# Kernel tuning notes

Hardware: AMD Instinct MI355X
Metric: run time of the kernel (lower is better)

## Reference

```python
import jax, jax.numpy as jnp
import numpy as np
from jax import lax

# QuantumDMRGLayer (isolated_labelnode=True) as a pure MPS chain contraction.
# Per sample: contract each site's (2,m[,m]) tensor with the 2-dim input vector
# over the physical leg, then multiply the resulting bond matrices along the
# chain, inserting the (m,m,nblabels) output tensor after site pos_label.

B, L, M, NBL = 2048, 196, 16, 10  # batch, dimvec, bond_len, nblabels


def setup_inputs() -> dict:
    key = jax.random.key(0)
    k_in, k_mid, k_l, k_r, k_out = jax.random.split(key, 5)
    # std chosen for numerical stability of a 196-long matrix product:
    # each site matrix is x0*A[0]+x1*A[1] with x~N(0,1), so effective per-site
    # gain ~ std*sqrt(2*m); std = 1/sqrt(2*m) keeps the product O(1).
    std = 1.0 / np.sqrt(2.0 * M)
    inputs = jax.random.normal(k_in, (B, L, 2), dtype=jnp.float32)
    eye2m = jnp.eye(M, dtype=jnp.float32)[:2, :]  # eye(max(2,m))[0:2,:] -> (2, m)
    A_left = eye2m + 1e-3 * jax.random.normal(k_l, (2, M), dtype=jnp.float32)
    A_right = eye2m + 1e-3 * jax.random.normal(k_r, (2, M), dtype=jnp.float32)
    A_mid = std * jax.random.normal(k_mid, (L - 2, 2, M, M), dtype=jnp.float32)
    T_out = (1.0 / np.sqrt(M)) * jax.random.normal(k_out, (M, M, NBL), dtype=jnp.float32)
    return {
        "inputs": inputs,
        "A_left": A_left,
        "A_mid": A_mid,
        "A_right": A_right,
        "T_out": T_out,
        "pos_label": 98,
    }


def reference(inputs, A_left, A_mid, A_right, T_out, pos_label):
    # Contract physical legs: interior site i (1..L-2) -> batched (m,m) matrix.
    mats = jnp.einsum("bsd,sdij->sbij", inputs[:, 1:-1, :], A_mid)  # (L-2, B, m, m)
    v_left = jnp.einsum("bd,dm->bm", inputs[:, 0, :], A_left)       # (B, m)
    v_right = jnp.einsum("bd,dm->bm", inputs[:, -1, :], A_right)    # (B, m)

    def step_l(v, Mx):  # v @ M, batched
        return jnp.einsum("bm,bmn->bn", v, Mx), None

    def step_r(v, Mx):  # M @ v, batched (sweep from the right end inward)
        return jnp.einsum("bmn,bn->bm", Mx, v), None

    # sites 1..pos_label feed the left bond of the output node,
    # sites pos_label+1..L-2 feed the right bond.
    left, _ = lax.scan(step_l, v_left, mats[:pos_label])
    right, _ = lax.scan(step_r, v_right, mats[pos_label:], reverse=True)
    return jnp.einsum("bm,mnl,bn->bl", left, T_out, right)  # (B, nblabels)
```

## Files before the change

kernel.cpp:

```cpp
#include <hip/hip_runtime.h>


typedef __attribute__((ext_vector_type(8))) short short8;
typedef __attribute__((ext_vector_type(16))) float floatx16;

#define GSITE_DW 512
#define GDIR_DW (100 * GSITE_DW)
#define STATE_DW (2 * GDIR_DW)

__device__ __forceinline__ unsigned bf16_rne(unsigned u) {
    return (u + 0x7FFFu + ((u >> 16) & 1u)) >> 16;
}

__global__ __launch_bounds__(256)
void prep_kernel(const float* __restrict__ AM, unsigned* __restrict__ WS)
{
    const int bid = blockIdx.x;
    const int dir = bid / 100;
    const int p   = bid % 100;
    const int lim = dir ? 96 : 98;
    const int a   = dir ? (193 - p) : p;
    const int t   = threadIdx.x;

    __shared__ float sM[512];
    if (p < lim)
        ((float2*)sM)[t] = ((const float2*)(AM + a * 512))[t];
    else
        ((float2*)sM)[t] = make_float2(0.f, 0.f);
    __syncthreads();

    const int w    = t & 3;
    const int lane = t >> 2;
    const int kb = (lane >> 5) << 3;
    const int r  = lane & 31;
    const int rr = (r & 0x13) | ((r & 4) << 1) | ((r & 8) >> 1);
    const int d = rr >> 4, nn = rr & 15;
    const int k0 = kb + 2 * w;

    float g0, g1;
    if (dir == 0) { g0 = sM[d * 256 + k0 * 16 + nn];
                    g1 = sM[d * 256 + (k0 + 1) * 16 + nn]; }
    else          { g0 = sM[d * 256 + nn * 16 + k0];
                    g1 = sM[d * 256 + nn * 16 + k0 + 1]; }

    const unsigned h0 = bf16_rne(__float_as_uint(g0));
    const unsigned h1 = bf16_rne(__float_as_uint(g1));
    const float l0f = g0 - __uint_as_float(h0 << 16);
    const float l1f = g1 - __uint_as_float(h1 << 16);
    const unsigned lo0 = bf16_rne(__float_as_uint(l0f));
    const unsigned lo1 = bf16_rne(__float_as_uint(l1f));

    unsigned* gp = WS + (dir * 100 + p) * GSITE_DW;
    gp[t]       = (h1 << 16) | h0;
    gp[256 + t] = (lo1 << 16) | lo0;
}

__global__ __launch_bounds__(64, 1)
void chain_kernel(const float* __restrict__ X,
                  const float* __restrict__ AL,
                  const float* __restrict__ AR,
                  const unsigned* __restrict__ WS,
                  float* __restrict__ WST)
{
    const int lane = threadIdx.x;
    const int dir  = blockIdx.x & 1;
    const int s    = (blockIdx.x >> 1) * 32 + (lane & 31);
    const int kb   = (lane >> 5) << 3;
    const float* Xs = X + s * 392;
    const unsigned* Gb = WS + dir * GDIR_DW + lane * 4;

    float w[8];
    int4 vh4, vl4;
    auto pack = [&]() {
#pragma unroll
        for (int q = 0; q < 4; ++q) {
            const unsigned u0 = __float_as_uint(w[2 * q]);
            const unsigned u1 = __float_as_uint(w[2 * q + 1]);
            const float l0 = w[2 * q]     - __uint_as_float(u0 & 0xFFFF0000u);
            const float l1 = w[2 * q + 1] - __uint_as_float(u1 & 0xFFFF0000u);
            ((unsigned*)&vh4)[q] = __builtin_amdgcn_perm(u1, u0, 0x07060302u);
            ((unsigned*)&vl4)[q] = __builtin_amdgcn_perm(
                __float_as_uint(l1), __float_as_uint(l0), 0x07060302u);
        }
    };

    const float* Ai = dir ? AR : AL;
    const float2 xi = *(const float2*)(Xs + (dir ? 390 : 0));
#pragma unroll
    for (int j = 0; j < 8; ++j)
        w[j] = xi.x * Ai[kb + j] + xi.y * Ai[16 + kb + j];
    pack();

    int4 GH[4], GL[4];
    float2 xr[4];
#pragma unroll
    for (int i = 0; i < 4; ++i) {
        GH[i] = *(const int4*)(Gb + i * GSITE_DW);
        GL[i] = *(const int4*)(Gb + i * GSITE_DW + 256);
        xr[i] = *(const float2*)(Xs + (dir ? (388 - 2 * i) : (2 + 2 * i)));
    }

    auto site = [&](int j4, bool pf, int pn) {
        const short8 ah = *(short8*)&GH[j4];
        const short8 al = *(short8*)&GL[j4];
        const short8 bh = *(short8*)&vh4;
        const short8 bl = *(short8*)&vl4;
        floatx16 Da = {}, Db = {};
        Da = __builtin_amdgcn_mfma_f32_32x32x16_bf16(ah, bh, Da, 0, 0, 0);
        Db = __builtin_amdgcn_mfma_f32_32x32x16_bf16(ah, bl, Db, 0, 0, 0);
        Db = __builtin_amdgcn_mfma_f32_32x32x16_bf16(al, bh, Db, 0, 0, 0);
        const float2 xs = xr[j4];
        if (pf) {
            GH[j4] = *(const int4*)(Gb + pn * GSITE_DW);
            GL[j4] = *(const int4*)(Gb + pn * GSITE_DW + 256);
            xr[j4] = *(const float2*)(Xs + (dir ? (388 - 2 * pn)
                                                : (2 + 2 * pn)));
        }
#pragma unroll
        for (int j = 0; j < 8; ++j)
            w[j] = fmaf(xs.x, Da[j] + Db[j], xs.y * (Da[j + 8] + Db[j + 8]));
        pack();
    };

    for (int c = 0; c < 24; ++c) {
#pragma unroll
        for (int j4 = 0; j4 < 4; ++j4)
            site(j4, true, 4 * c + j4 + 4);
    }
    if (dir == 0) {
        site(0, false, 0);
        site(1, false, 0);
    }

    float* st = WST + (dir * 2048 + s) * 16 + kb;
    *(float4*)(st)     = make_float4(w[0], w[1], w[2], w[3]);
    *(float4*)(st + 4) = make_float4(w[4], w[5], w[6], w[7]);
}

__global__ __launch_bounds__(256)
void out_kernel(const float* __restrict__ T, const float* __restrict__ WST,
                float* __restrict__ OUT)
{
    __shared__ float sT[2560];
    const int tid = threadIdx.x;
    for (int k = tid; k < 640; k += 256)
        ((float4*)sT)[k] = ((const float4*)T)[k];
    __syncthreads();
    const int t = blockIdx.x * 256 + tid;
    const int s = t / 10, l = t - s * 10;
    const float* L = WST + s * 16;
    const float* R = WST + 2048 * 16 + s * 16;
    const float4 Ra = *(const float4*)(R);
    const float4 Rb = *(const float4*)(R + 4);
    const float4 Rc = *(const float4*)(R + 8);
    const float4 Rd = *(const float4*)(R + 12);
    float acc = 0.f;
#pragma unroll
    for (int m = 0; m < 16; ++m) {
        const float lm = L[m];
        const float* Tp = sT + m * 160 + l;
        acc = fmaf(lm * Ra.x, Tp[0],   acc);
        acc = fmaf(lm * Ra.y, Tp[10],  acc);
        acc = fmaf(lm * Ra.z, Tp[20],  acc);
        acc = fmaf(lm * Ra.w, Tp[30],  acc);
        acc = fmaf(lm * Rb.x, Tp[40],  acc);
        acc = fmaf(lm * Rb.y, Tp[50],  acc);
        acc = fmaf(lm * Rb.z, Tp[60],  acc);
        acc = fmaf(lm * Rb.w, Tp[70],  acc);
        acc = fmaf(lm * Rc.x, Tp[80],  acc);
        acc = fmaf(lm * Rc.y, Tp[90],  acc);
        acc = fmaf(lm * Rc.z, Tp[100], acc);
        acc = fmaf(lm * Rc.w, Tp[110], acc);
        acc = fmaf(lm * Rd.x, Tp[120], acc);
        acc = fmaf(lm * Rd.y, Tp[130], acc);
        acc = fmaf(lm * Rd.z, Tp[140], acc);
        acc = fmaf(lm * Rd.w, Tp[150], acc);
    }
    OUT[t] = acc;
}

extern "C" void kernel_launch(void* const* d_in, const int* in_sizes, int n_in,
                              void* d_out, int out_size, void* d_ws, size_t ws_size,
                              hipStream_t stream)
{
    const float* X  = (const float*)d_in[0];
    const float* AL = (const float*)d_in[1];
    const float* AM = (const float*)d_in[2];
    const float* AR = (const float*)d_in[3];
    const float* T  = (const float*)d_in[4];
    (void)in_sizes; (void)n_in; (void)out_size; (void)ws_size;
    unsigned* WS = (unsigned*)d_ws;
    float* WST   = (float*)d_ws + STATE_DW;
    float* OUT   = (float*)d_out;

    hipLaunchKernelGGL(prep_kernel,  dim3(200), dim3(256), 0, stream, AM, WS);
    hipLaunchKernelGGL(chain_kernel, dim3(128), dim3(64),  0, stream,
                       X, AL, AR, WS, WST);
    hipLaunchKernelGGL(out_kernel,   dim3(80),  dim3(256), 0, stream,
                       T, WST, OUT);
}
```

Measured before the change: 89.68 us.

## Fuse output contraction into chain kernel and pack both directions per block

Merges the out_kernel into the chain kernel. Each 128-thread block now runs the left and right sweeps for 32 samples as two waves, exchanges the final bond vectors through shared memory, and contracts them with a transposed copy of T staged in LDS. The site update math is rewritten with 2-wide float vectors to encourage packed FMA instructions. This removes one kernel launch and the workspace round trip. In exchange it halves the block count, to 64 CUs with two waves each, and adds a serial epilogue plus T staging to the critical path.

```diff
diff --git a/kernel.cpp b/kernel.cpp
--- a/kernel.cpp
+++ b/kernel.cpp
@@ -3,10 +3,10 @@
 
 typedef __attribute__((ext_vector_type(8))) short short8;
 typedef __attribute__((ext_vector_type(16))) float floatx16;
+typedef __attribute__((ext_vector_type(2))) float float2v;
 
 #define GSITE_DW 512
 #define GDIR_DW (100 * GSITE_DW)
-#define STATE_DW (2 * GDIR_DW)
 
 __device__ __forceinline__ unsigned bf16_rne(unsigned u) {
     return (u + 0x7FFFu + ((u >> 16) & 1u)) >> 16;
@@ -55,41 +55,57 @@
     gp[256 + t] = (lo1 << 16) | lo0;
 }
 
-__global__ __launch_bounds__(64, 1)
+__global__ __launch_bounds__(128, 1)
 void chain_kernel(const float* __restrict__ X,
                   const float* __restrict__ AL,
                   const float* __restrict__ AR,
+                  const float* __restrict__ T,
                   const unsigned* __restrict__ WS,
-                  float* __restrict__ WST)
+                  float* __restrict__ OUT)
 {
-    const int lane = threadIdx.x;
-    const int dir  = blockIdx.x & 1;
-    const int s    = (blockIdx.x >> 1) * 32 + (lane & 31);
+    __shared__ float sTt[2560];
+    __shared__ float sS[2][32][16];
+
+    const int tid  = threadIdx.x;
+    const int dir  = tid >> 6;
+    const int lane = tid & 63;
+    const int sl   = lane & 31;
     const int kb   = (lane >> 5) << 3;
+    const int s    = (int)blockIdx.x * 32 + sl;
     const float* Xs = X + s * 392;
     const unsigned* Gb = WS + dir * GDIR_DW + lane * 4;
 
-    float w[8];
+    for (int k = tid; k < 2560; k += 128) {
+        const int m = k / 160, rem = k - m * 160;
+        const int n = rem / 10, l = rem - n * 10;
+        sTt[l * 256 + m * 16 + n] = T[k];
+    }
+
+    float2v w2[4];
     int4 vh4, vl4;
-    auto pack = [&]() {
+    auto packv = [&]() {
 #pragma unroll
         for (int q = 0; q < 4; ++q) {
-            const unsigned u0 = __float_as_uint(w[2 * q]);
-            const unsigned u1 = __float_as_uint(w[2 * q + 1]);
-            const float l0 = w[2 * q]     - __uint_as_float(u0 & 0xFFFF0000u);
-            const float l1 = w[2 * q + 1] - __uint_as_float(u1 & 0xFFFF0000u);
+            const unsigned u0 = __float_as_uint(w2[q].x);
+            const unsigned u1 = __float_as_uint(w2[q].y);
+            float2v hi;
+            hi.x = __uint_as_float(u0 & 0xFFFF0000u);
+            hi.y = __uint_as_float(u1 & 0xFFFF0000u);
+            const float2v lo = w2[q] - hi;
             ((unsigned*)&vh4)[q] = __builtin_amdgcn_perm(u1, u0, 0x07060302u);
             ((unsigned*)&vl4)[q] = __builtin_amdgcn_perm(
-                __float_as_uint(l1), __float_as_uint(l0), 0x07060302u);
+                __float_as_uint(lo.y), __float_as_uint(lo.x), 0x07060302u);
         }
     };
 
     const float* Ai = dir ? AR : AL;
     const float2 xi = *(const float2*)(Xs + (dir ? 390 : 0));
 #pragma unroll
-    for (int j = 0; j < 8; ++j)
-        w[j] = xi.x * Ai[kb + j] + xi.y * Ai[16 + kb + j];
-    pack();
+    for (int q = 0; q < 4; ++q) {
+        w2[q].x = xi.x * Ai[kb + 2 * q]     + xi.y * Ai[16 + kb + 2 * q];
+        w2[q].y = xi.x * Ai[kb + 2 * q + 1] + xi.y * Ai[16 + kb + 2 * q + 1];
+    }
+    packv();
 
     int4 GH[4], GL[4];
     float2 xr[4];
@@ -116,10 +132,18 @@
             xr[j4] = *(const float2*)(Xs + (dir ? (388 - 2 * pn)
                                                 : (2 + 2 * pn)));
         }
-#pragma unroll
-        for (int j = 0; j < 8; ++j)
-            w[j] = fmaf(xs.x, Da[j] + Db[j], xs.y * (Da[j + 8] + Db[j + 8]));
-        pack();
+        const float2v xx = {xs.x, xs.x}, xy = {xs.y, xs.y};
+#pragma unroll
+        for (int q = 0; q < 4; ++q) {
+            const float2v da = {Da[2 * q],     Da[2 * q + 1]};
+            const float2v db = {Db[2 * q],     Db[2 * q + 1]};
+            const float2v ea = {Da[2 * q + 8], Da[2 * q + 9]};
+            const float2v eb = {Db[2 * q + 8], Db[2 * q + 9]};
+            const float2v s0 = da + db;
+            const float2v s1 = ea + eb;
+            w2[q] = __builtin_elementwise_fma(xx, s0, xy * s1);
+        }
+        packv();
     };
 
     for (int c = 0; c < 24; ++c) {
@@ -132,51 +156,47 @@
         site(1, false, 0);
     }
 
-    float* st = WST + (dir * 2048 + s) * 16 + kb;
-    *(float4*)(st)     = make_float4(w[0], w[1], w[2], w[3]);
-    *(float4*)(st + 4) = make_float4(w[4], w[5], w[6], w[7]);
-}
-
-__global__ __launch_bounds__(256)
-void out_kernel(const float* __restrict__ T, const float* __restrict__ WST,
-                float* __restrict__ OUT)
-{
-    __shared__ float sT[2560];
-    const int tid = threadIdx.x;
-    for (int k = tid; k < 640; k += 256)
-        ((float4*)sT)[k] = ((const float4*)T)[k];
+#pragma unroll
+    for (int q = 0; q < 4; ++q)
+        *(float2*)&sS[dir][sl][kb + 2 * q] = make_float2(w2[q].x, w2[q].y);
     __syncthreads();
-    const int t = blockIdx.x * 256 + tid;
-    const int s = t / 10, l = t - s * 10;
-    const float* L = WST + s * 16;
-    const float* R = WST + 2048 * 16 + s * 16;
-    const float4 Ra = *(const float4*)(R);
-    const float4 Rb = *(const float4*)(R + 4);
-    const float4 Rc = *(const float4*)(R + 8);
-    const float4 Rd = *(const float4*)(R + 12);
-    float acc = 0.f;
-#pragma unroll
-    for (int m = 0; m < 16; ++m) {
-        const float lm = L[m];
-        const float* Tp = sT + m * 160 + l;
-        acc = fmaf(lm * Ra.x, Tp[0],   acc);
-        acc = fmaf(lm * Ra.y, Tp[10],  acc);
-        acc = fmaf(lm * Ra.z, Tp[20],  acc);
-        acc = fmaf(lm * Ra.w, Tp[30],  acc);
-        acc = fmaf(lm * Rb.x, Tp[40],  acc);
-        acc = fmaf(lm * Rb.y, Tp[50],  acc);
-        acc = fmaf(lm * Rb.z, Tp[60],  acc);
-        acc = fmaf(lm * Rb.w, Tp[70],  acc);
-        acc = fmaf(lm * Rc.x, Tp[80],  acc);
-        acc = fmaf(lm * Rc.y, Tp[90],  acc);
-        acc = fmaf(lm * Rc.z, Tp[100], acc);
-        acc = fmaf(lm * Rc.w, Tp[110], acc);
-        acc = fmaf(lm * Rd.x, Tp[120], acc);
-        acc = fmaf(lm * Rd.y, Tp[130], acc);
-        acc = fmaf(lm * Rd.z, Tp[140], acc);
-        acc = fmaf(lm * Rd.w, Tp[150], acc);
-    }
-    OUT[t] = acc;
+
+    for (int o = tid; o < 320; o += 128) {
+        const int sm = o / 10, l = o - sm * 10;
+        const float* L = sS[0][sm];
+        const float* R = sS[1][sm];
+        const float4 Ra = *(const float4*)(R);
+        const float4 Rb = *(const float4*)(R + 4);
+        const float4 Rc = *(const float4*)(R + 8);
+        const float4 Rd = *(const float4*)(R + 12);
+        const float* Tp = sTt + l * 256;
+        float acc = 0.f;
+#pragma unroll
+        for (int m = 0; m < 16; ++m) {
+            const float lm = L[m];
+            const float4 t0 = *(const float4*)(Tp + m * 16);
+            const float4 t1 = *(const float4*)(Tp + m * 16 + 4);
+            const float4 t2 = *(const float4*)(Tp + m * 16 + 8);
+            const float4 t3 = *(const float4*)(Tp + m * 16 + 12);
+            acc = fmaf(lm * Ra.x, t0.x, acc);
+            acc = fmaf(lm * Ra.y, t0.y, acc);
+            acc = fmaf(lm * Ra.z, t0.z, acc);
+            acc = fmaf(lm * Ra.w, t0.w, acc);
+            acc = fmaf(lm * Rb.x, t1.x, acc);
+            acc = fmaf(lm * Rb.y, t1.y, acc);
+            acc = fmaf(lm * Rb.z, t1.z, acc);
+            acc = fmaf(lm * Rb.w, t1.w, acc);
+            acc = fmaf(lm * Rc.x, t2.x, acc);
+            acc = fmaf(lm * Rc.y, t2.y, acc);
+            acc = fmaf(lm * Rc.z, t2.z, acc);
+            acc = fmaf(lm * Rc.w, t2.w, acc);
+            acc = fmaf(lm * Rd.x, t3.x, acc);
+            acc = fmaf(lm * Rd.y, t3.y, acc);
+            acc = fmaf(lm * Rd.z, t3.z, acc);
+            acc = fmaf(lm * Rd.w, t3.w, acc);
+        }
+        OUT[((int)blockIdx.x * 32 + sm) * 10 + l] = acc;
+    }
 }
 
 extern "C" void kernel_launch(void* const* d_in, const int* in_sizes, int n_in,
@@ -190,12 +210,9 @@
     const float* T  = (const float*)d_in[4];
     (void)in_sizes; (void)n_in; (void)out_size; (void)ws_size;
     unsigned* WS = (unsigned*)d_ws;
-    float* WST   = (float*)d_ws + STATE_DW;
     float* OUT   = (float*)d_out;
 
     hipLaunchKernelGGL(prep_kernel,  dim3(200), dim3(256), 0, stream, AM, WS);
-    hipLaunchKernelGGL(chain_kernel, dim3(128), dim3(64),  0, stream,
-                       X, AL, AR, WS, WST);
-    hipLaunchKernelGGL(out_kernel,   dim3(80),  dim3(256), 0, stream,
-                       T, WST, OUT);
-}
+    hipLaunchKernelGGL(chain_kernel, dim3(64),  dim3(128), 0, stream,
+                       X, AL, AR, T, WS, OUT);
+}
```

After: 92.27 us. +2.9%, slower.

## Pre-multiply adjacent site tensors pairwise to halve sequential chain steps

Applied to the files above, without the earlier changes.

The prep kernel now multiplies each pair of adjacent site tensors into four 16x16 products per physical-index combination (d1,d2). The chain then advances two sites per step using six independent MFMAs combined with the outer product of the two input vectors. This halves the length of the serial dependency chain and lets the MFMAs overlap, at the cost of more MFMA work per step, more register traffic, and rounding the fused product to bf16 hi/lo.

```diff
diff --git a/kernel.cpp b/kernel.cpp
--- a/kernel.cpp
+++ b/kernel.cpp
@@ -3,9 +3,10 @@
 
 typedef __attribute__((ext_vector_type(8))) short short8;
 typedef __attribute__((ext_vector_type(16))) float floatx16;
-
-#define GSITE_DW 512
-#define GDIR_DW (100 * GSITE_DW)
+typedef __attribute__((ext_vector_type(2))) float float2v;
+
+#define PAIR_DW 1024
+#define GDIR_DW (50 * PAIR_DW)
 #define STATE_DW (2 * GDIR_DW)
 
 __device__ __forceinline__ unsigned bf16_rne(unsigned u) {
@@ -16,17 +17,23 @@
 void prep_kernel(const float* __restrict__ AM, unsigned* __restrict__ WS)
 {
     const int bid = blockIdx.x;
-    const int dir = bid / 100;
-    const int p   = bid % 100;
-    const int lim = dir ? 96 : 98;
-    const int a   = dir ? (193 - p) : p;
+    const int dir = bid / 50;
+    const int q   = bid % 50;
     const int t   = threadIdx.x;
 
-    __shared__ float sM[512];
-    if (p < lim)
-        ((float2*)sM)[t] = ((const float2*)(AM + a * 512))[t];
-    else
-        ((float2*)sM)[t] = make_float2(0.f, 0.f);
+    __shared__ float sF[512];
+    __shared__ float sS[512];
+
+    int i0, i1; bool valid;
+    if (dir == 0) { i0 = 2 * q;       i1 = 2 * q + 1;   valid = (q < 49); }
+    else          { i0 = 193 - 2 * q; i1 = 192 - 2 * q; valid = (q < 48); }
+    if (valid) {
+        ((float2*)sF)[t] = ((const float2*)(AM + i0 * 512))[t];
+        ((float2*)sS)[t] = ((const float2*)(AM + i1 * 512))[t];
+    } else {
+        ((float2*)sF)[t] = make_float2(0.f, 0.f);
+        ((float2*)sS)[t] = make_float2(0.f, 0.f);
+    }
     __syncthreads();
 
     const int w    = t & 3;
@@ -37,22 +44,49 @@
     const int d = rr >> 4, nn = rr & 15;
     const int k0 = kb + 2 * w;
 
-    float g0, g1;
-    if (dir == 0) { g0 = sM[d * 256 + k0 * 16 + nn];
-                    g1 = sM[d * 256 + (k0 + 1) * 16 + nn]; }
-    else          { g0 = sM[d * 256 + nn * 16 + k0];
-                    g1 = sM[d * 256 + nn * 16 + k0 + 1]; }
-
-    const unsigned h0 = bf16_rne(__float_as_uint(g0));
-    const unsigned h1 = bf16_rne(__float_as_uint(g1));
-    const float l0f = g0 - __uint_as_float(h0 << 16);
-    const float l1f = g1 - __uint_as_float(h1 << 16);
-    const unsigned lo0 = bf16_rne(__float_as_uint(l0f));
-    const unsigned lo1 = bf16_rne(__float_as_uint(l1f));
-
-    unsigned* gp = WS + (dir * 100 + p) * GSITE_DW;
-    gp[t]       = (h1 << 16) | h0;
-    gp[256 + t] = (lo1 << 16) | lo0;
+    float g10 = 0.f, g11 = 0.f, g20 = 0.f, g21 = 0.f;
+    if (dir == 0) {
+#pragma unroll
+        for (int u = 0; u < 16; ++u) {
+            const float s2 = sS[d * 256 + u * 16 + nn];
+            g10 = fmaf(sF[      k0 * 16 + u],       s2, g10);
+            g11 = fmaf(sF[      (k0 + 1) * 16 + u], s2, g11);
+            g20 = fmaf(sF[256 + k0 * 16 + u],       s2, g20);
+            g21 = fmaf(sF[256 + (k0 + 1) * 16 + u], s2, g21);
+        }
+    } else {
+#pragma unroll
+        for (int u = 0; u < 16; ++u) {
+            const float f0 = sF[d * 256 + u * 16 + k0];
+            const float f1 = sF[d * 256 + u * 16 + k0 + 1];
+            const float a0 = sS[      nn * 16 + u];
+            const float a1 = sS[256 + nn * 16 + u];
+            g10 = fmaf(a0, f0, g10);  g11 = fmaf(a0, f1, g11);
+            g20 = fmaf(a1, f0, g20);  g21 = fmaf(a1, f1, g21);
+        }
+    }
+
+    unsigned* gp = WS + (dir * 50 + q) * PAIR_DW;
+    {
+        const unsigned h0 = bf16_rne(__float_as_uint(g10));
+        const unsigned h1 = bf16_rne(__float_as_uint(g11));
+        const unsigned l0 = bf16_rne(__float_as_uint(
+            g10 - __uint_as_float(h0 << 16)));
+        const unsigned l1 = bf16_rne(__float_as_uint(
+            g11 - __uint_as_float(h1 << 16)));
+        gp[t]       = (h1 << 16) | h0;
+        gp[256 + t] = (l1 << 16) | l0;
+    }
+    {
+        const unsigned h0 = bf16_rne(__float_as_uint(g20));
+        const unsigned h1 = bf16_rne(__float_as_uint(g21));
+        const unsigned l0 = bf16_rne(__float_as_uint(
+            g20 - __uint_as_float(h0 << 16)));
+        const unsigned l1 = bf16_rne(__float_as_uint(
+            g21 - __uint_as_float(h1 << 16)));
+        gp[512 + t] = (h1 << 16) | h0;
+        gp[768 + t] = (l1 << 16) | l0;
+    }
 }
 
 __global__ __launch_bounds__(64, 1)
@@ -69,72 +103,101 @@
     const float* Xs = X + s * 392;
     const unsigned* Gb = WS + dir * GDIR_DW + lane * 4;
 
-    float w[8];
+    float2v w2[4];
     int4 vh4, vl4;
-    auto pack = [&]() {
+    auto packv = [&]() {
 #pragma unroll
         for (int q = 0; q < 4; ++q) {
-            const unsigned u0 = __float_as_uint(w[2 * q]);
-            const unsigned u1 = __float_as_uint(w[2 * q + 1]);
-            const float l0 = w[2 * q]     - __uint_as_float(u0 & 0xFFFF0000u);
-            const float l1 = w[2 * q + 1] - __uint_as_float(u1 & 0xFFFF0000u);
+            const unsigned u0 = __float_as_uint(w2[q].x);
+            const unsigned u1 = __float_as_uint(w2[q].y);
+            float2v hi;
+            hi.x = __uint_as_float(u0 & 0xFFFF0000u);
+            hi.y = __uint_as_float(u1 & 0xFFFF0000u);
+            const float2v lo = w2[q] - hi;
             ((unsigned*)&vh4)[q] = __builtin_amdgcn_perm(u1, u0, 0x07060302u);
             ((unsigned*)&vl4)[q] = __builtin_amdgcn_perm(
-                __float_as_uint(l1), __float_as_uint(l0), 0x07060302u);
+                __float_as_uint(lo.y), __float_as_uint(lo.x), 0x07060302u);
         }
     };
 
     const float* Ai = dir ? AR : AL;
     const float2 xi = *(const float2*)(Xs + (dir ? 390 : 0));
 #pragma unroll
-    for (int j = 0; j < 8; ++j)
-        w[j] = xi.x * Ai[kb + j] + xi.y * Ai[16 + kb + j];
-    pack();
-
-    int4 GH[4], GL[4];
-    float2 xr[4];
-#pragma unroll
-    for (int i = 0; i < 4; ++i) {
-        GH[i] = *(const int4*)(Gb + i * GSITE_DW);
-        GL[i] = *(const int4*)(Gb + i * GSITE_DW + 256);
-        xr[i] = *(const float2*)(Xs + (dir ? (388 - 2 * i) : (2 + 2 * i)));
-    }
-
-    auto site = [&](int j4, bool pf, int pn) {
-        const short8 ah = *(short8*)&GH[j4];
-        const short8 al = *(short8*)&GL[j4];
+    for (int q = 0; q < 4; ++q) {
+        w2[q].x = xi.x * Ai[kb + 2 * q]     + xi.y * Ai[16 + kb + 2 * q];
+        w2[q].y = xi.x * Ai[kb + 2 * q + 1] + xi.y * Ai[16 + kb + 2 * q + 1];
+    }
+    packv();
+
+    auto xoffA = [&](int p) { return dir ? (386 - 4 * p) : (4 * p + 2); };
+    auto xoffB = [&](int p) { return dir ? (388 - 4 * p) : (4 * p + 4); };
+
+    int4 G1H[2], G1L[2], G2H[2], G2L[2];
+    float2 xa[2], xb[2];
+#pragma unroll
+    for (int i = 0; i < 2; ++i) {
+        const unsigned* gp = Gb + i * PAIR_DW;
+        G1H[i] = *(const int4*)(gp);
+        G1L[i] = *(const int4*)(gp + 256);
+        G2H[i] = *(const int4*)(gp + 512);
+        G2L[i] = *(const int4*)(gp + 768);
+        xa[i] = *(const float2*)(Xs + xoffA(i));
+        xb[i] = *(const float2*)(Xs + xoffB(i));
+    }
+
+    auto pair_step = [&](int sl, bool pf, int pn) {
+        const short8 a1h = *(short8*)&G1H[sl];
+        const short8 a1l = *(short8*)&G1L[sl];
+        const short8 a2h = *(short8*)&G2H[sl];
+        const short8 a2l = *(short8*)&G2L[sl];
         const short8 bh = *(short8*)&vh4;
         const short8 bl = *(short8*)&vl4;
-        floatx16 Da = {}, Db = {};
-        Da = __builtin_amdgcn_mfma_f32_32x32x16_bf16(ah, bh, Da, 0, 0, 0);
-        Db = __builtin_amdgcn_mfma_f32_32x32x16_bf16(ah, bl, Db, 0, 0, 0);
-        Db = __builtin_amdgcn_mfma_f32_32x32x16_bf16(al, bh, Db, 0, 0, 0);
-        const float2 xs = xr[j4];
+        floatx16 Da1 = {}, Db1 = {}, Da2 = {}, Db2 = {};
+        Da1 = __builtin_amdgcn_mfma_f32_32x32x16_bf16(a1h, bh, Da1, 0, 0, 0);
+        Da2 = __builtin_amdgcn_mfma_f32_32x32x16_bf16(a2h, bh, Da2, 0, 0, 0);
+        Db1 = __builtin_amdgcn_mfma_f32_32x32x16_bf16(a1h, bl, Db1, 0, 0, 0);
+        Db2 = __builtin_amdgcn_mfma_f32_32x32x16_bf16(a2h, bl, Db2, 0, 0, 0);
+        Db1 = __builtin_amdgcn_mfma_f32_32x32x16_bf16(a1l, bh, Db1, 0, 0, 0);
+        Db2 = __builtin_amdgcn_mfma_f32_32x32x16_bf16(a2l, bh, Db2, 0, 0, 0);
+        const float2 va = xa[sl], vb = xb[sl];
         if (pf) {
-            GH[j4] = *(const int4*)(Gb + pn * GSITE_DW);
-            GL[j4] = *(const int4*)(Gb + pn * GSITE_DW + 256);
-            xr[j4] = *(const float2*)(Xs + (dir ? (388 - 2 * pn)
-                                                : (2 + 2 * pn)));
-        }
-#pragma unroll
-        for (int j = 0; j < 8; ++j)
-            w[j] = fmaf(xs.x, Da[j] + Db[j], xs.y * (Da[j + 8] + Db[j + 8]));
-        pack();
+            const unsigned* gp = Gb + pn * PAIR_DW;
+            G1H[sl] = *(const int4*)(gp);
+            G1L[sl] = *(const int4*)(gp + 256);
+            G2H[sl] = *(const int4*)(gp + 512);
+            G2L[sl] = *(const int4*)(gp + 768);
+            xa[sl] = *(const float2*)(Xs + xoffA(pn));
+            xb[sl] = *(const float2*)(Xs + xoffB(pn));
+        }
+        const float2v C00 = {va.x * vb.x, va.x * vb.x};
+        const float2v C01 = {va.x * vb.y, va.x * vb.y};
+        const float2v C10 = {va.y * vb.x, va.y * vb.x};
+        const float2v C11 = {va.y * vb.y, va.y * vb.y};
+#pragma unroll
+        for (int q = 0; q < 4; ++q) {
+            const float2v s1l = float2v{Da1[2*q],   Da1[2*q+1]} +
+                                float2v{Db1[2*q],   Db1[2*q+1]};
+            const float2v s1h = float2v{Da1[2*q+8], Da1[2*q+9]} +
+                                float2v{Db1[2*q+8], Db1[2*q+9]};
+            const float2v s2l = float2v{Da2[2*q],   Da2[2*q+1]} +
+                                float2v{Db2[2*q],   Db2[2*q+1]};
+            const float2v s2h = float2v{Da2[2*q+8], Da2[2*q+9]} +
+                                float2v{Db2[2*q+8], Db2[2*q+9]};
+            w2[q] = __builtin_elementwise_fma(C00, s1l,
+                    __builtin_elementwise_fma(C01, s1h,
+                    __builtin_elementwise_fma(C10, s2l, C11 * s2h)));
+        }
+        packv();
     };
 
-    for (int c = 0; c < 24; ++c) {
-#pragma unroll
-        for (int j4 = 0; j4 < 4; ++j4)
-            site(j4, true, 4 * c + j4 + 4);
-    }
-    if (dir == 0) {
-        site(0, false, 0);
-        site(1, false, 0);
-    }
+    for (int p = 0; p < 48; ++p)
+        pair_step(p & 1, true, p + 2);
+    if (dir == 0)
+        pair_step(0, false, 0);
 
     float* st = WST + (dir * 2048 + s) * 16 + kb;
-    *(float4*)(st)     = make_float4(w[0], w[1], w[2], w[3]);
-    *(float4*)(st + 4) = make_float4(w[4], w[5], w[6], w[7]);
+    *(float4*)(st)     = make_float4(w2[0].x, w2[0].y, w2[1].x, w2[1].y);
+    *(float4*)(st + 4) = make_float4(w2[2].x, w2[2].y, w2[3].x, w2[3].y);
 }
 
 __global__ __launch_bounds__(256)
@@ -193,7 +256,7 @@
     float* WST   = (float*)d_ws + STATE_DW;
     float* OUT   = (float*)d_out;
 
-    hipLaunchKernelGGL(prep_kernel,  dim3(200), dim3(256), 0, stream, AM, WS);
+    hipLaunchKernelGGL(prep_kernel,  dim3(100), dim3(256), 0, stream, AM, WS);
     hipLaunchKernelGGL(chain_kernel, dim3(128), dim3(64),  0, stream,
                        X, AL, AR, WS, WST);
     hipLaunchKernelGGL(out_kernel,   dim3(80),  dim3(256), 0, stream,
```

Result: slower. 111.6 us (+24.5%).

## Split each chain sweep into two halves with identity-started partial products

Applied to the files above, without the earlier changes.

Each direction's sequential chain is split in two. The outer half is propagated from the boundary vector as before. The inner half is computed as a full 16x16 partial product, started from identity basis vectors in extra blocks (2048 extra blocks per direction). The output kernel then multiplies the boundary vectors by the partial matrices before the final tensor contraction. This halves the serial MFMA dependency chain per block and raises the block count from 128 to 2176, so the GPU has more work to run in parallel. The cost is extra total work, a large intermediate buffer in workspace, and some packed-float math in the per-site update.

```diff
diff --git a/kernel.cpp b/kernel.cpp
--- a/kernel.cpp
+++ b/kernel.cpp
@@ -3,10 +3,14 @@
 
 typedef __attribute__((ext_vector_type(8))) short short8;
 typedef __attribute__((ext_vector_type(16))) float floatx16;
+typedef __attribute__((ext_vector_type(2))) float float2v;
 
 #define GSITE_DW 512
 #define GDIR_DW (100 * GSITE_DW)
-#define STATE_DW (2 * GDIR_DW)
+#define L1OFF (2 * GDIR_DW)
+#define R1OFF (L1OFF + 2048 * 16)
+#define PLOFF (R1OFF + 2048 * 16)
+#define PROFF (PLOFF + 2048 * 256)
 
 __device__ __forceinline__ unsigned bf16_rne(unsigned u) {
     return (u + 0x7FFFu + ((u >> 16) & 1u)) >> 16;
@@ -60,36 +64,56 @@
                   const float* __restrict__ AL,
                   const float* __restrict__ AR,
                   const unsigned* __restrict__ WS,
-                  float* __restrict__ WST)
+                  float* __restrict__ WSF)
 {
     const int lane = threadIdx.x;
-    const int dir  = blockIdx.x & 1;
-    const int s    = (blockIdx.x >> 1) * 32 + (lane & 31);
+    const int c    = lane & 31;
     const int kb   = (lane >> 5) << 3;
+
+    int bid = blockIdx.x, mode, dir, g;
+    if (bid < 128) { mode = 0; dir = bid >> 6;  g = bid & 63; }
+    else { bid -= 128; mode = 1; dir = bid >> 10; g = bid & 1023; }
+    const int p0 = mode ? (dir ? 48 : 49) : 0;
+    const int s  = mode ? (g * 2 + (c >> 4)) : (g * 32 + c);
+    const int b  = c & 15;
     const float* Xs = X + s * 392;
-    const unsigned* Gb = WS + dir * GDIR_DW + lane * 4;
-
-    float w[8];
+    const unsigned* Gb = WS + dir * GDIR_DW + p0 * GSITE_DW + lane * 4;
+
+    float2v w2[4];
     int4 vh4, vl4;
-    auto pack = [&]() {
-#pragma unroll
-        for (int q = 0; q < 4; ++q) {
-            const unsigned u0 = __float_as_uint(w[2 * q]);
-            const unsigned u1 = __float_as_uint(w[2 * q + 1]);
-            const float l0 = w[2 * q]     - __uint_as_float(u0 & 0xFFFF0000u);
-            const float l1 = w[2 * q + 1] - __uint_as_float(u1 & 0xFFFF0000u);
+    auto packv = [&]() {
+#pragma unroll
+        for (int q = 0; q < 4; ++q) {
+            const unsigned u0 = __float_as_uint(w2[q].x);
+            const unsigned u1 = __float_as_uint(w2[q].y);
+            float2v hi;
+            hi.x = __uint_as_float(u0 & 0xFFFF0000u);
+            hi.y = __uint_as_float(u1 & 0xFFFF0000u);
+            const float2v lo = w2[q] - hi;
             ((unsigned*)&vh4)[q] = __builtin_amdgcn_perm(u1, u0, 0x07060302u);
             ((unsigned*)&vl4)[q] = __builtin_amdgcn_perm(
-                __float_as_uint(l1), __float_as_uint(l0), 0x07060302u);
+                __float_as_uint(lo.y), __float_as_uint(lo.x), 0x07060302u);
         }
     };
 
-    const float* Ai = dir ? AR : AL;
-    const float2 xi = *(const float2*)(Xs + (dir ? 390 : 0));
-#pragma unroll
-    for (int j = 0; j < 8; ++j)
-        w[j] = xi.x * Ai[kb + j] + xi.y * Ai[16 + kb + j];
-    pack();
+    if (mode == 0) {
+        const float* Ai = dir ? AR : AL;
+        const float2 xi = *(const float2*)(Xs + (dir ? 390 : 0));
+#pragma unroll
+        for (int q = 0; q < 4; ++q) {
+            w2[q].x = xi.x * Ai[kb + 2 * q]     + xi.y * Ai[16 + kb + 2 * q];
+            w2[q].y = xi.x * Ai[kb + 2 * q + 1] + xi.y * Ai[16 + kb + 2 * q + 1];
+        }
+    } else {
+#pragma unroll
+        for (int q = 0; q < 4; ++q) {
+            w2[q].x = (kb + 2 * q     == b) ? 1.f : 0.f;
+            w2[q].y = (kb + 2 * q + 1 == b) ? 1.f : 0.f;
+        }
+    }
+    packv();
+
+    auto xoff = [&](int p) { return dir ? (388 - 2 * p) : (2 * p + 2); };
 
     int4 GH[4], GL[4];
     float2 xr[4];
@@ -97,10 +121,10 @@
     for (int i = 0; i < 4; ++i) {
         GH[i] = *(const int4*)(Gb + i * GSITE_DW);
         GL[i] = *(const int4*)(Gb + i * GSITE_DW + 256);
-        xr[i] = *(const float2*)(Xs + (dir ? (388 - 2 * i) : (2 + 2 * i)));
-    }
-
-    auto site = [&](int j4, bool pf, int pn) {
+        xr[i] = *(const float2*)(Xs + xoff(p0 + i));
+    }
+
+    auto site = [&](int j4, bool pf, int pr) {
         const short8 ah = *(short8*)&GH[j4];
         const short8 al = *(short8*)&GL[j4];
         const short8 bh = *(short8*)&vh4;
@@ -111,72 +135,102 @@
         Db = __builtin_amdgcn_mfma_f32_32x32x16_bf16(al, bh, Db, 0, 0, 0);
         const float2 xs = xr[j4];
         if (pf) {
-            GH[j4] = *(const int4*)(Gb + pn * GSITE_DW);
-            GL[j4] = *(const int4*)(Gb + pn * GSITE_DW + 256);
-            xr[j4] = *(const float2*)(Xs + (dir ? (388 - 2 * pn)
-                                                : (2 + 2 * pn)));
-        }
-#pragma unroll
-        for (int j = 0; j < 8; ++j)
-            w[j] = fmaf(xs.x, Da[j] + Db[j], xs.y * (Da[j + 8] + Db[j + 8]));
-        pack();
+            GH[j4] = *(const int4*)(Gb + pr * GSITE_DW);
+            GL[j4] = *(const int4*)(Gb + pr * GSITE_DW + 256);
+            xr[j4] = *(const float2*)(Xs + xoff(p0 + pr));
+        }
+        const float2v xx = {xs.x, xs.x}, xy = {xs.y, xs.y};
+#pragma unroll
+        for (int q = 0; q < 4; ++q) {
+            const float2v s0 = float2v{Da[2*q],   Da[2*q+1]} +
+                               float2v{Db[2*q],   Db[2*q+1]};
+            const float2v s1 = float2v{Da[2*q+8], Da[2*q+9]} +
+                               float2v{Db[2*q+8], Db[2*q+9]};
+            w2[q] = __builtin_elementwise_fma(xx, s0, xy * s1);
+        }
+        packv();
     };
 
-    for (int c = 0; c < 24; ++c) {
+    for (int cc = 0; cc < 12; ++cc) {
 #pragma unroll
         for (int j4 = 0; j4 < 4; ++j4)
-            site(j4, true, 4 * c + j4 + 4);
-    }
-    if (dir == 0) {
+            site(j4, true, 4 * cc + j4 + 4);
+    }
+    if (dir == 0)
         site(0, false, 0);
-        site(1, false, 0);
-    }
-
-    float* st = WST + (dir * 2048 + s) * 16 + kb;
-    *(float4*)(st)     = make_float4(w[0], w[1], w[2], w[3]);
-    *(float4*)(st + 4) = make_float4(w[4], w[5], w[6], w[7]);
+
+    float* dst;
+    if (mode == 0) dst = WSF + (dir ? R1OFF : L1OFF) + s * 16 + kb;
+    else           dst = WSF + (dir ? PROFF : PLOFF) + s * 256 + b * 16 + kb;
+    *(float4*)(dst)     = make_float4(w2[0].x, w2[0].y, w2[1].x, w2[1].y);
+    *(float4*)(dst + 4) = make_float4(w2[2].x, w2[2].y, w2[3].x, w2[3].y);
 }
 
 __global__ __launch_bounds__(256)
-void out_kernel(const float* __restrict__ T, const float* __restrict__ WST,
+void out_kernel(const float* __restrict__ T, const float* __restrict__ WSF,
                 float* __restrict__ OUT)
 {
     __shared__ float sT[2560];
+    __shared__ float sL1[1024], sR1[1024];
+    __shared__ float sL[1024],  sR[1024];
     const int tid = threadIdx.x;
+    const int s0  = (int)blockIdx.x * 64;
+
     for (int k = tid; k < 640; k += 256)
         ((float4*)sT)[k] = ((const float4*)T)[k];
+    for (int k = tid; k < 1024; k += 256) {
+        sL1[k] = WSF[L1OFF + s0 * 16 + k];
+        sR1[k] = WSF[R1OFF + s0 * 16 + k];
+    }
     __syncthreads();
-    const int t = blockIdx.x * 256 + tid;
-    const int s = t / 10, l = t - s * 10;
-    const float* L = WST + s * 16;
-    const float* R = WST + 2048 * 16 + s * 16;
-    const float4 Ra = *(const float4*)(R);
-    const float4 Rb = *(const float4*)(R + 4);
-    const float4 Rc = *(const float4*)(R + 8);
-    const float4 Rd = *(const float4*)(R + 12);
-    float acc = 0.f;
-#pragma unroll
-    for (int m = 0; m < 16; ++m) {
-        const float lm = L[m];
-        const float* Tp = sT + m * 160 + l;
-        acc = fmaf(lm * Ra.x, Tp[0],   acc);
-        acc = fmaf(lm * Ra.y, Tp[10],  acc);
-        acc = fmaf(lm * Ra.z, Tp[20],  acc);
-        acc = fmaf(lm * Ra.w, Tp[30],  acc);
-        acc = fmaf(lm * Rb.x, Tp[40],  acc);
-        acc = fmaf(lm * Rb.y, Tp[50],  acc);
-        acc = fmaf(lm * Rb.z, Tp[60],  acc);
-        acc = fmaf(lm * Rb.w, Tp[70],  acc);
-        acc = fmaf(lm * Rc.x, Tp[80],  acc);
-        acc = fmaf(lm * Rc.y, Tp[90],  acc);
-        acc = fmaf(lm * Rc.z, Tp[100], acc);
-        acc = fmaf(lm * Rc.w, Tp[110], acc);
-        acc = fmaf(lm * Rd.x, Tp[120], acc);
-        acc = fmaf(lm * Rd.y, Tp[130], acc);
-        acc = fmaf(lm * Rd.z, Tp[140], acc);
-        acc = fmaf(lm * Rd.w, Tp[150], acc);
-    }
-    OUT[t] = acc;
+
+    for (int it = tid; it < 1024; it += 256) {
+        const int sl = it >> 4, k = it & 15;
+        const float* PLs = WSF + PLOFF + (size_t)(s0 + sl) * 256 + k;
+        const float* PRs = WSF + PROFF + (size_t)(s0 + sl) * 256 + k;
+        float accL = 0.f, accR = 0.f;
+#pragma unroll
+        for (int bb = 0; bb < 16; ++bb) {
+            accL = fmaf(sL1[sl * 16 + bb], PLs[bb * 16], accL);
+            accR = fmaf(sR1[sl * 16 + bb], PRs[bb * 16], accR);
+        }
+        sL[it] = accL;
+        sR[it] = accR;
+    }
+    __syncthreads();
+
+    for (int o = tid; o < 640; o += 256) {
+        const int sl = o / 10, l = o - sl * 10;
+        const float* L = sL + sl * 16;
+        const float* R = sR + sl * 16;
+        const float4 Ra = *(const float4*)(R);
+        const float4 Rb = *(const float4*)(R + 4);
+        const float4 Rc = *(const float4*)(R + 8);
+        const float4 Rd = *(const float4*)(R + 12);
+        float acc = 0.f;
+#pragma unroll
+        for (int m = 0; m < 16; ++m) {
+            const float lm = L[m];
+            const float* Tp = sT + m * 160 + l;
+            acc = fmaf(lm * Ra.x, Tp[0],   acc);
+            acc = fmaf(lm * Ra.y, Tp[10],  acc);
+            acc = fmaf(lm * Ra.z, Tp[20],  acc);
+            acc = fmaf(lm * Ra.w, Tp[30],  acc);
+            acc = fmaf(lm * Rb.x, Tp[40],  acc);
+            acc = fmaf(lm * Rb.y, Tp[50],  acc);
+            acc = fmaf(lm * Rb.z, Tp[60],  acc);
+            acc = fmaf(lm * Rb.w, Tp[70],  acc);
+            acc = fmaf(lm * Rc.x, Tp[80],  acc);
+            acc = fmaf(lm * Rc.y, Tp[90],  acc);
+            acc = fmaf(lm * Rc.z, Tp[100], acc);
+            acc = fmaf(lm * Rc.w, Tp[110], acc);
+            acc = fmaf(lm * Rd.x, Tp[120], acc);
+            acc = fmaf(lm * Rd.y, Tp[130], acc);
+            acc = fmaf(lm * Rd.z, Tp[140], acc);
+            acc = fmaf(lm * Rd.w, Tp[150], acc);
+        }
+        OUT[(s0 + sl) * 10 + l] = acc;
+    }
 }
 
 extern "C" void kernel_launch(void* const* d_in, const int* in_sizes, int n_in,
@@ -190,12 +244,12 @@
     const float* T  = (const float*)d_in[4];
     (void)in_sizes; (void)n_in; (void)out_size; (void)ws_size;
     unsigned* WS = (unsigned*)d_ws;
-    float* WST   = (float*)d_ws + STATE_DW;
+    float* WSF   = (float*)d_ws;
     float* OUT   = (float*)d_out;
 
-    hipLaunchKernelGGL(prep_kernel,  dim3(200), dim3(256), 0, stream, AM, WS);
-    hipLaunchKernelGGL(chain_kernel, dim3(128), dim3(64),  0, stream,
-                       X, AL, AR, WS, WST);
-    hipLaunchKernelGGL(out_kernel,   dim3(80),  dim3(256), 0, stream,
-                       T, WST, OUT);
-}
+    hipLaunchKernelGGL(prep_kernel,  dim3(200),  dim3(256), 0, stream, AM, WS);
+    hipLaunchKernelGGL(chain_kernel, dim3(2176), dim3(64),  0, stream,
+                       X, AL, AR, WS, WSF);
+    hipLaunchKernelGGL(out_kernel,   dim3(32),   dim3(256), 0, stream,
+                       T, WSF, OUT);
+}
```

After: 108.8 us. 1.21x slower.
